# Kernel tuning notes

Measured on AMD Instinct MI355X. Metric: run time of the kernel, lower is better.

## Reference

```python
import jax, jax.numpy as jnp
import numpy as np

L, B, S, D, H, V = 6, 4, 1024, 1024, 16, 32000
HD = D // H          # head_size = 64
F = 4 * D            # ffn hidden
EPS = 1e-5           # nn.LayerNorm default


def setup_inputs() -> dict:
    key = jax.random.key(0)
    ks = jax.random.split(key, 12)
    s = 0.02
    p = {
        "tokens": jax.random.randint(ks[0], (B, S), 0, V, dtype=jnp.int32),
        "tok_emb": s * jax.random.normal(ks[1], (V, D), jnp.float32),
        "pos_emb": s * jax.random.normal(ks[2], (S, D), jnp.float32),
        # stacked per-layer params (leading dim L)
        "Wq": s * jax.random.normal(ks[3], (L, D, D), jnp.float32),
        "Wk": s * jax.random.normal(ks[4], (L, D, D), jnp.float32),
        "Wv": s * jax.random.normal(ks[5], (L, D, D), jnp.float32),
        "Wp": s * jax.random.normal(ks[6], (L, D, D), jnp.float32),
        "ln1_s": jnp.ones((L, D), jnp.float32),
        "ln1_b": jnp.zeros((L, D), jnp.float32),
        "W1": s * jax.random.normal(ks[7], (L, D, F), jnp.float32),
        "b1": jnp.zeros((L, F), jnp.float32),
        "W2": s * jax.random.normal(ks[8], (L, F, D), jnp.float32),
        "b2": jnp.zeros((L, D), jnp.float32),
        "ln2_s": jnp.ones((L, D), jnp.float32),
        "ln2_b": jnp.zeros((L, D), jnp.float32),
        "lnf_s": jnp.ones((D,), jnp.float32),
        "lnf_b": jnp.zeros((D,), jnp.float32),
        "Wh": s * jax.random.normal(ks[9], (D, V), jnp.float32),
        "bh": jnp.zeros((V,), jnp.float32),
    }
    return p


def _ln(x, scale, bias):
    m = x.mean(-1, keepdims=True)
    v = ((x - m) ** 2).mean(-1, keepdims=True)
    return (x - m) * jax.lax.rsqrt(v + EPS) * scale + bias


def reference(tokens, tok_emb, pos_emb, Wq, Wk, Wv, Wp, ln1_s, ln1_b,
              W1, b1, W2, b2, ln2_s, ln2_b, lnf_s, lnf_b, Wh, bh):
    x = tok_emb[tokens] + pos_emb[None, :, :]            # [B,S,D]
    mask = jnp.tril(jnp.ones((S, S), dtype=bool))
    inv_sqrt_hd = HD ** -0.5

    def layer(x, p):
        wq, wk, wv, wp, l1s, l1b, w1, b1_, w2, b2_, l2s, l2b = p
        q = jnp.einsum('bsd,dhk->bhsk', x, wq.reshape(D, H, HD))
        k = jnp.einsum('bsd,dhk->bhsk', x, wk.reshape(D, H, HD))
        v = jnp.einsum('bsd,dhk->bhsk', x, wv.reshape(D, H, HD))
        scores = jnp.einsum('bhsk,bhtk->bhst', q, k)     # [B,H,S,S]
        # original: masked_fill(-inf) THEN * head_size**-0.5 (same math: -inf stays -inf)
        scores = jnp.where(mask, scores * inv_sqrt_hd, -jnp.inf)
        attn = jax.nn.softmax(scores, axis=-1)
        o = jnp.einsum('bhst,bhtk->bhsk', attn, v)
        o = o.transpose(0, 2, 1, 3).reshape(B, S, D) @ wp
        a = x + _ln(o, l1s, l1b)                          # residual + ln1 (as in source)
        f = jax.nn.relu(a @ w1 + b1_) @ w2 + b2_
        return x + _ln(f, l2s, l2b), None                 # residual from block INPUT (as in source)

    x, _ = jax.lax.scan(layer, x,
                        (Wq, Wk, Wv, Wp, ln1_s, ln1_b, W1, b1, W2, b2, ln2_s, ln2_b))
    return _ln(x, lnf_s, lnf_b) @ Wh + bh                 # [B,S,V]
```

## Files before the change

kernel.cpp:

```cpp
#include <hip/hip_runtime.h>

#define DEV __device__ __forceinline__

typedef __attribute__((ext_vector_type(4))) float f32x4;
typedef __attribute__((ext_vector_type(8))) short short8_t;

constexpr int LNUM = 6;
constexpr int BB = 4;
constexpr int SS = 1024;
constexpr int DD = 1024;
constexpr int HH = 16;
constexpr int HDD = 64;
constexpr int FF = 4096;
constexpr int VV = 32000;
constexpr int MROWS = BB * SS;

DEV short f2bf(float f) {
  union { float f; unsigned u; } x; x.f = f;
  unsigned r = x.u + 0x7fffu + ((x.u >> 16) & 1u);
  return (short)(r >> 16);
}

DEV float bf2f(short s) {
  union { unsigned u; float f; } x;
  x.u = ((unsigned)(unsigned short)s) << 16;
  return x.f;
}

#define BAR() do { __builtin_amdgcn_sched_barrier(0); \
  __builtin_amdgcn_s_barrier(); \
  __builtin_amdgcn_sched_barrier(0); } while (0)

__global__ __launch_bounds__(256) void k_embed(
    const int* __restrict__ tok, const float* __restrict__ te,
    const float* __restrict__ pe, float* __restrict__ xf,
    short* __restrict__ xb) {
  int i = blockIdx.x * 256 + threadIdx.x;
  int bs = i >> 8, d4 = i & 255;
  int t = tok[bs];
  float4 a = ((const float4*)(te + (size_t)t * DD))[d4];
  float4 b = ((const float4*)(pe + (size_t)(bs & (SS - 1)) * DD))[d4];
  float4 r; r.x = a.x + b.x; r.y = a.y + b.y; r.z = a.z + b.z; r.w = a.w + b.w;
  ((float4*)xf)[i] = r;
  short4 o; o.x = f2bf(r.x); o.y = f2bf(r.y); o.z = f2bf(r.z); o.w = f2bf(r.w);
  ((short4*)xb)[i] = o;
}

__global__ __launch_bounds__(256) void k_tcvt4(
    const float* __restrict__ in, short* __restrict__ out, int K, int N,
    long long istride, long long ostride) {
  __shared__ float tile[64][65];
  const float* ip = in + (size_t)blockIdx.z * istride;
  short* op = out + (size_t)blockIdx.z * ostride;
  const int bn = blockIdx.x * 64, bk = blockIdx.y * 64;
  const int tc = threadIdx.x & 15, tr = threadIdx.x >> 4;
  #pragma unroll
  for (int i = 0; i < 4; i++) {
    const int r = tr + 16 * i;
    float4 v = *(const float4*)&ip[(size_t)(bk + r) * N + bn + tc * 4];
    tile[r][tc * 4 + 0] = v.x; tile[r][tc * 4 + 1] = v.y;
    tile[r][tc * 4 + 2] = v.z; tile[r][tc * 4 + 3] = v.w;
  }
  __syncthreads();
  #pragma unroll
  for (int i = 0; i < 4; i++) {
    const int wr = tr + 16 * i;
    short4 s;
    s.x = f2bf(tile[tc * 4 + 0][wr]);
    s.y = f2bf(tile[tc * 4 + 1][wr]);
    s.z = f2bf(tile[tc * 4 + 2][wr]);
    s.w = f2bf(tile[tc * 4 + 3][wr]);
    *(short4*)&op[(size_t)(bn + wr) * K + bk + tc * 4] = s;
  }
}

__global__ __launch_bounds__(256) void k_tcvt4q(
    const float* __restrict__ Wq, const float* __restrict__ Wk,
    const float* __restrict__ Wv, short* __restrict__ out) {
  __shared__ float tile[64][65];
  const int z = blockIdx.z, l = z / 3, which = z - l * 3;
  const float* ip = (which == 0 ? Wq : which == 1 ? Wk : Wv)
                    + (size_t)l * DD * DD;
  short* op = out + (size_t)z * DD * DD;
  const int bn = blockIdx.x * 64, bk = blockIdx.y * 64;
  const int tc = threadIdx.x & 15, tr = threadIdx.x >> 4;
  #pragma unroll
  for (int i = 0; i < 4; i++) {
    const int r = tr + 16 * i;
    float4 v = *(const float4*)&ip[(size_t)(bk + r) * DD + bn + tc * 4];
    tile[r][tc * 4 + 0] = v.x; tile[r][tc * 4 + 1] = v.y;
    tile[r][tc * 4 + 2] = v.z; tile[r][tc * 4 + 3] = v.w;
  }
  __syncthreads();
  #pragma unroll
  for (int i = 0; i < 4; i++) {
    const int wr = tr + 16 * i;
    short4 s;
    s.x = f2bf(tile[tc * 4 + 0][wr]);
    s.y = f2bf(tile[tc * 4 + 1][wr]);
    s.z = f2bf(tile[tc * 4 + 2][wr]);
    s.w = f2bf(tile[tc * 4 + 3][wr]);
    *(short4*)&op[(size_t)(bn + wr) * DD + bk + tc * 4] = s;
  }
}

DEV void gload16(const short* g, short* l) {
  __builtin_amdgcn_global_load_lds(
      (const __attribute__((address_space(1))) void*)g,
      (__attribute__((address_space(3))) void*)l, 16, 0, 0);
}

template<int MODE>
DEV void gemm256_body(short* lds,
    const short* __restrict__ A, const short* __restrict__ Bt,
    const float* __restrict__ bias, void* __restrict__ Cp,
    int M, int N, int K, int lda, int ldb) {
  const int tid = threadIdx.x;
  const int nbx = gridDim.x;
  const int nwg = nbx << 4;
  const int hid = blockIdx.y * nbx + blockIdx.x;
  const int cpx = nwg >> 3;
  const int lid = (hid & 7) * cpx + (hid >> 3);
  const int bx = lid >> 4, by = lid & 15;
  const int n0 = bx * 256, m0 = by * 256;

  const int lane = tid & 63;
  const int wid = tid >> 6;
  const int wm = wid >> 2, wn = wid & 3;
  const int l16 = lane & 15, kg = lane >> 4;
  const int xorv = (l16 & 7) << 4;
  const int cs[2] = { ((kg << 4) ^ xorv) >> 1,
                      ((64 | (kg << 4)) ^ xorv) >> 1 };
  const int rr = tid >> 3;
  const int sce = ((((tid & 7) << 4) ^ ((rr & 7) << 4)) >> 1);
  const int ldst = (tid & ~63) * 8;

  const int NT = K >> 6;

  auto stageA = [&](int t2, int c2) {
    const int k0 = t2 << 6;
    const int base = c2 * 32768;
    #pragma unroll
    for (int h = 0; h < 2; h++)
      #pragma unroll
      for (int li = 0; li < 2; li++)
        gload16(A + (size_t)(m0 + h * 128 + li * 64 + rr) * lda + k0 + sce,
                &lds[base + h * 8192 + li * 4096 + ldst]);
  };
  auto stageB = [&](int t2, int c2) {
    const int k0 = t2 << 6;
    const int base = c2 * 32768 + 16384;
    #pragma unroll
    for (int h = 0; h < 2; h++)
      #pragma unroll
      for (int li = 0; li < 2; li++)
        gload16(Bt + (size_t)(n0 + h * 128 + li * 64 + rr) * ldb + k0 + sce,
                &lds[base + h * 8192 + li * 4096 + ldst]);
  };

  f32x4 acc[8][4];
  #pragma unroll
  for (int mi = 0; mi < 8; mi++)
    #pragma unroll
    for (int ni = 0; ni < 4; ni++)
      #pragma unroll
      for (int j = 0; j < 4; j++) acc[mi][ni][j] = 0.f;

  auto storeQ = [&](int mlo, int nlo) {
    #pragma unroll
    for (int mi = 0; mi < 4; mi++)
      #pragma unroll
      for (int ni = 0; ni < 2; ni++)
        #pragma unroll
        for (int j = 0; j < 4; j++) {
          const int r = m0 + wm * 128 + (mlo + mi) * 16 + kg * 4 + j;
          const int c = n0 + wn * 64 + (nlo + ni) * 16 + l16;
          ((float*)Cp)[(size_t)r * N + c] = acc[mlo + mi][nlo + ni][j] + bias[c];
        }
  };

  stageA(0, 0); stageB(0, 0);
  stageA(1, 1); stageB(1, 1);
  asm volatile("s_waitcnt vmcnt(8)" ::: "memory");
  BAR();

  for (int t = 0; t < NT; t++) {
    const int c = t & 1;
    const int ao = c * 32768 + wm * 8192;
    const int bo = c * 32768 + 16384 + (wn >> 1) * 8192 + (wn & 1) * 4096;
    short8_t a[4][2], b0[2][2], b1[2][2];

    #pragma unroll
    for (int mi = 0; mi < 4; mi++)
      #pragma unroll
      for (int kk = 0; kk < 2; kk++)
        a[mi][kk] = *(const short8_t*)&lds[ao + (mi * 16 + l16) * 64 + cs[kk]];
    #pragma unroll
    for (int ni = 0; ni < 2; ni++)
      #pragma unroll
      for (int kk = 0; kk < 2; kk++)
        b0[ni][kk] = *(const short8_t*)&lds[bo + (ni * 16 + l16) * 64 + cs[kk]];
    BAR();
    __builtin_amdgcn_s_setprio(1);
    #pragma unroll
    for (int mi = 0; mi < 4; mi++)
      #pragma unroll
      for (int ni = 0; ni < 2; ni++)
        #pragma unroll
        for (int kk = 0; kk < 2; kk++)
          acc[mi][ni] = __builtin_amdgcn_mfma_f32_16x16x32_bf16(
              a[mi][kk], b0[ni][kk], acc[mi][ni], 0, 0, 0);
    __builtin_amdgcn_s_setprio(0);
    if (MODE == 9 && t == NT - 1) storeQ(0, 0);
    BAR();

    #pragma unroll
    for (int ni = 0; ni < 2; ni++)
      #pragma unroll
      for (int kk = 0; kk < 2; kk++)
        b1[ni][kk] = *(const short8_t*)&lds[bo + ((ni + 2) * 16 + l16) * 64 + cs[kk]];
    BAR();
    __builtin_amdgcn_s_setprio(1);
    #pragma unroll
    for (int mi = 0; mi < 4; mi++)
      #pragma unroll
      for (int ni = 0; ni < 2; ni++)
        #pragma unroll
        for (int kk = 0; kk < 2; kk++)
          acc[mi][ni + 2] = __builtin_amdgcn_mfma_f32_16x16x32_bf16(
              a[mi][kk], b1[ni][kk], acc[mi][ni + 2], 0, 0, 0);
    __builtin_amdgcn_s_setprio(0);
    if (MODE == 9 && t == NT - 1) storeQ(0, 2);
    BAR();

    #pragma unroll
    for (int mi = 0; mi < 4; mi++)
      #pragma unroll
      for (int kk = 0; kk < 2; kk++)
        a[mi][kk] = *(const short8_t*)&lds[ao + ((mi + 4) * 16 + l16) * 64 + cs[kk]];
    if (t + 2 < NT) stageB(t + 2, c);
    BAR();
    __builtin_amdgcn_s_setprio(1);
    #pragma unroll
    for (int mi = 0; mi < 4; mi++)
      #pragma unroll
      for (int ni = 0; ni < 2; ni++)
        #pragma unroll
        for (int kk = 0; kk < 2; kk++)
          acc[mi + 4][ni + 2] = __builtin_amdgcn_mfma_f32_16x16x32_bf16(
              a[mi][kk], b1[ni][kk], acc[mi + 4][ni + 2], 0, 0, 0);
    __builtin_amdgcn_s_setprio(0);
    if (MODE == 9 && t == NT - 1) storeQ(4, 2);
    BAR();

    if (t + 2 < NT) stageA(t + 2, c);
    BAR();
    __builtin_amdgcn_s_setprio(1);
    #pragma unroll
    for (int mi = 0; mi < 4; mi++)
      #pragma unroll
      for (int ni = 0; ni < 2; ni++)
        #pragma unroll
        for (int kk = 0; kk < 2; kk++)
          acc[mi + 4][ni] = __builtin_amdgcn_mfma_f32_16x16x32_bf16(
              a[mi][kk], b0[ni][kk], acc[mi + 4][ni], 0, 0, 0);
    __builtin_amdgcn_s_setprio(0);
    if (t + 2 < NT) asm volatile("s_waitcnt vmcnt(8)" ::: "memory");
    else            asm volatile("s_waitcnt vmcnt(0)" ::: "memory");
    BAR();
  }

  if (MODE == 9) {
    storeQ(4, 0);
    return;
  }
  #pragma unroll
  for (int mi = 0; mi < 8; mi++) {
    #pragma unroll
    for (int ni = 0; ni < 4; ni++) {
      #pragma unroll
      for (int j = 0; j < 4; j++) {
        const int r = m0 + wm * 128 + mi * 16 + kg * 4 + j;
        const int c = n0 + wn * 64 + ni * 16 + l16;
        const float v = acc[mi][ni][j];
        if (MODE == 6) {
          ((short*)Cp)[(size_t)r * N + c] = f2bf(fmaxf(v + bias[c], 0.f));
        } else if (MODE == 8) {
          int kind = c >> 10, cc = c & 1023;
          int b = r >> 10, s = r & 1023, h = cc >> 6, hd = cc & 63;
          size_t off;
          if (kind < 2)
            off = (size_t)kind * MROWS * DD +
                  (((size_t)(b * HH + h) << 10) + s) * HDD + hd;
          else
            off = (size_t)2 * MROWS * DD +
                  (((size_t)(b * HH + h) * HDD + hd) << 10) + s;
          ((short*)Cp)[off] = f2bf(v);
        }
      }
    }
  }
}

__global__ __launch_bounds__(512, 2) void k_qkv(
    const short* __restrict__ A, const short* __restrict__ Bt,
    const float* __restrict__ bias, void* __restrict__ Cp,
    int M, int N, int K, int lda, int ldb) {
  extern __shared__ short lds[];
  gemm256_body<8>(lds, A, Bt, bias, Cp, M, N, K, lda, ldb);
}
__global__ __launch_bounds__(512, 2) void k_ffn1(
    const short* __restrict__ A, const short* __restrict__ Bt,
    const float* __restrict__ bias, void* __restrict__ Cp,
    int M, int N, int K, int lda, int ldb) {
  extern __shared__ short lds[];
  gemm256_body<6>(lds, A, Bt, bias, Cp, M, N, K, lda, ldb);
}
__global__ __launch_bounds__(512, 2) void k_logits(
    const short* __restrict__ A, const short* __restrict__ Bt,
    const float* __restrict__ bias, void* __restrict__ Cp,
    int M, int N, int K, int lda, int ldb) {
  extern __shared__ short lds[];
  gemm256_body<9>(lds, A, Bt, bias, Cp, M, N, K, lda, ldb);
}

template<int MODE>
DEV void gemm128db_body(short* lds,
    const short* __restrict__ A, const short* __restrict__ Bt,
    const float* __restrict__ bias, void* __restrict__ Cp,
    int M, int N, int K, int lda, int ldb) {
  const int tid = threadIdx.x;
  const int n0 = blockIdx.x * 128, m0 = blockIdx.y * 128;
  const int lane = tid & 63;
  const int wid = tid >> 6;
  const int wm = wid >> 1, wn = wid & 1;
  const int l16 = lane & 15, kg = lane >> 4;
  const int xorv = (l16 & 7) << 4;
  const int cs[2] = { ((kg << 4) ^ xorv) >> 1,
                      ((64 | (kg << 4)) ^ xorv) >> 1 };
  const int rr = tid >> 3;
  const int sce = ((((tid & 7) << 4) ^ ((rr & 7) << 4)) >> 1);
  const int ldst = (tid & ~63) * 8;

  const int NT = K >> 6;

  auto stage = [&](int t2, int c2) {
    const int k0 = t2 << 6;
    const int base = c2 * 16384;
    #pragma unroll
    for (int i = 0; i < 4; i++)
      gload16(A + (size_t)(m0 + i * 32 + rr) * lda + k0 + sce,
              &lds[base + i * 2048 + ldst]);
    #pragma unroll
    for (int i = 0; i < 4; i++)
      gload16(Bt + (size_t)(n0 + i * 32 + rr) * ldb + k0 + sce,
              &lds[base + 8192 + i * 2048 + ldst]);
  };

  f32x4 acc[4][4];
  #pragma unroll
  for (int a = 0; a < 4; a++)
    #pragma unroll
    for (int b = 0; b < 4; b++)
      #pragma unroll
      for (int j = 0; j < 4; j++) acc[a][b][j] = 0.f;

  stage(0, 0);
  asm volatile("s_waitcnt vmcnt(0)" ::: "memory");
  BAR();

  for (int t = 0; t < NT; t++) {
    const int c = t & 1;
    if (t + 1 < NT) stage(t + 1, c ^ 1);
    const int ab = c * 16384;
    short8_t a[4][2], b[4][2];
    #pragma unroll
    for (int mi = 0; mi < 4; mi++)
      #pragma unroll
      for (int kk = 0; kk < 2; kk++)
        a[mi][kk] = *(const short8_t*)
            &lds[ab + (wm * 64 + mi * 16 + l16) * 64 + cs[kk]];
    #pragma unroll
    for (int ni = 0; ni < 4; ni++)
      #pragma unroll
      for (int kk = 0; kk < 2; kk++)
        b[ni][kk] = *(const short8_t*)
            &lds[ab + 8192 + (wn * 64 + ni * 16 + l16) * 64 + cs[kk]];
    __builtin_amdgcn_s_setprio(1);
    #pragma unroll
    for (int mi = 0; mi < 4; mi++)
      #pragma unroll
      for (int ni = 0; ni < 4; ni++)
        #pragma unroll
        for (int kk = 0; kk < 2; kk++)
          acc[mi][ni] = __builtin_amdgcn_mfma_f32_16x16x32_bf16(
              a[mi][kk], b[ni][kk], acc[mi][ni], 0, 0, 0);
    __builtin_amdgcn_s_setprio(0);
    if (t + 1 < NT) asm volatile("s_waitcnt vmcnt(0)" ::: "memory");
    BAR();
  }

  #pragma unroll
  for (int mi = 0; mi < 4; mi++) {
    #pragma unroll
    for (int ni = 0; ni < 4; ni++) {
      #pragma unroll
      for (int j = 0; j < 4; j++) {
        const int r = m0 + wm * 64 + mi * 16 + kg * 4 + j;
        const int c = n0 + wn * 64 + ni * 16 + l16;
        const float v = acc[mi][ni][j];
        if (MODE == 15) {
          ((short*)Cp)[(size_t)r * N + c] = f2bf(v);
        } else if (MODE == 17) {
          ((short*)Cp)[(size_t)r * N + c] = f2bf(v + bias[c]);
        }
      }
    }
  }
}

__global__ __launch_bounds__(256, 2) void k_proj(
    const short* __restrict__ A, const short* __restrict__ Bt,
    const float* __restrict__ bias, void* __restrict__ Cp,
    int M, int N, int K, int lda, int ldb) {
  extern __shared__ short lds[];
  gemm128db_body<15>(lds, A, Bt, bias, Cp, M, N, K, lda, ldb);
}
__global__ __launch_bounds__(256, 2) void k_ffn2(
    const short* __restrict__ A, const short* __restrict__ Bt,
    const float* __restrict__ bias, void* __restrict__ Cp,
    int M, int N, int K, int lda, int ldb) {
  extern __shared__ short lds[];
  gemm128db_body<17>(lds, A, Bt, bias, Cp, M, N, K, lda, ldb);
}

#define RDSWZ(arr, r, cb) \
  (*(const short8_t*)&arr[((r) << 6) + ((((cb) ^ (((r) & 7) << 4))) >> 1)])
#define RDSWZ7(arr, r, cb) \
  (*(const short8_t*)&arr[((r) << 7) + ((((cb) ^ (((r) & 7) << 4))) >> 1)])

__global__ __launch_bounds__(512, 2) void k_attn(
    const short* __restrict__ Qg, const short* __restrict__ Kgl,
    const short* __restrict__ Vt, short* __restrict__ Og) {
  extern __shared__ short sm[];
  short* lP = sm + 32768;
  const int tid = threadIdx.x;
  const int z = blockIdx.y;
  const int qb = (z < 32) ? blockIdx.x : 7 - blockIdx.x;
  const int q0 = qb << 7;
  const short* Qp = Qg + ((size_t)z << 16);
  const short* Kp = Kgl + ((size_t)z << 16);
  const short* Vp = Vt + ((size_t)z << 16);
  const int bidx = z >> 4, h = z & 15;
  const int lane = tid & 63, w = tid >> 6;
  const int l16 = lane & 15, kg = lane >> 4;
  const int sr = tid >> 3;
  const int scb = ((((tid & 7) << 4) ^ ((sr & 7) << 4)) >> 1);
  const int vr = tid >> 4;
  const int vcb = ((((tid & 15) << 4) ^ ((vr & 7) << 4)) >> 1);
  const int ldst = (tid & ~63) << 3;

  auto stageK = [&](int kt, int c) {
    const int k0 = kt << 7;
    short* dst = sm + c * 16384;
    #pragma unroll
    for (int i = 0; i < 2; i++)
      gload16(Kp + ((size_t)(k0 + i * 64 + sr) << 6) + scb,
              dst + i * 4096 + ldst);
  };
  auto stageV = [&](int kt, int c) {
    const int k0 = kt << 7;
    short* dst = sm + c * 16384 + 8192;
    #pragma unroll
    for (int i = 0; i < 2; i++)
      gload16(Vp + ((size_t)(i * 32 + vr) << 10) + k0 + vcb,
              dst + i * 4096 + ldst);
  };

  #pragma unroll
  for (int i = 0; i < 2; i++)
    gload16(Qp + ((size_t)(q0 + i * 64 + sr) << 6) + scb,
            sm + 16384 + i * 4096 + ldst);
  __syncthreads();
  short8_t aq[2];
  #pragma unroll
  for (int kk = 0; kk < 2; kk++)
    aq[kk] = RDSWZ((sm + 16384), w * 16 + l16, kk * 64 + kg * 16);
  __syncthreads();

  f32x4 acc_o[4];
  float m_r[4], l_r[4];
  #pragma unroll
  for (int j = 0; j < 4; j++) {
    m_r[j] = -3e38f; l_r[j] = 0.f;
    #pragma unroll
    for (int n2 = 0; n2 < 4; n2++) acc_o[n2][j] = 0.f;
  }

  const float C = 0.125f * 1.44269504f;
  const int nkt = qb + 1;
  stageK(0, 0); stageV(0, 0);

  for (int kt = 0; kt < nkt; kt++) {
    const int cur = kt & 1;
    if (kt + 1 < nkt) {
      stageK(kt + 1, cur ^ 1); stageV(kt + 1, cur ^ 1);
      asm volatile("s_waitcnt vmcnt(4)" ::: "memory");
    } else {
      asm volatile("s_waitcnt vmcnt(0)" ::: "memory");
    }
    BAR();

    const short* lK = sm + cur * 16384;
    const short* lV = sm + cur * 16384 + 8192;
    const int k0 = kt << 7;

    f32x4 s[8];
    #pragma unroll
    for (int nf = 0; nf < 8; nf++)
      #pragma unroll
      for (int j = 0; j < 4; j++) s[nf][j] = 0.f;
    #pragma unroll
    for (int kk = 0; kk < 2; kk++)
      #pragma unroll
      for (int nf = 0; nf < 8; nf++) {
        short8_t bk = RDSWZ(lK, nf * 16 + l16, kk * 64 + kg * 16);
        s[nf] = __builtin_amdgcn_mfma_f32_16x16x32_bf16(aq[kk], bk, s[nf], 0, 0, 0);
      }

    const bool diag = (kt == qb);
    #pragma unroll
    for (int j = 0; j < 4; j++) {
      const int ql = w * 16 + kg * 4 + j;
      const int q = q0 + ql;
      float sv[8]; float tm = -3e38f;
      #pragma unroll
      for (int nf = 0; nf < 8; nf++) {
        const int kv = k0 + nf * 16 + l16;
        const float x = s[nf][j] * C;
        sv[nf] = (!diag || kv <= q) ? x : -3e38f;
        tm = fmaxf(tm, sv[nf]);
      }
      #pragma unroll
      for (int o = 1; o < 16; o <<= 1) tm = fmaxf(tm, __shfl_xor(tm, o));
      const float mn = fmaxf(m_r[j], tm);
      const float scale = exp2f(m_r[j] - mn);
      float ts = 0.f;
      #pragma unroll
      for (int nf = 0; nf < 8; nf++) {
        const float e = exp2f(sv[nf] - mn);
        ts += e;
        lP[(ql << 7) + ((nf * 16 + l16) ^ ((ql & 7) << 3))] = f2bf(e);
      }
      #pragma unroll
      for (int o = 1; o < 16; o <<= 1) ts += __shfl_xor(ts, o);
      l_r[j] = l_r[j] * scale + ts;
      m_r[j] = mn;
      #pragma unroll
      for (int n2 = 0; n2 < 4; n2++) acc_o[n2][j] *= scale;
    }

    #pragma unroll
    for (int kc = 0; kc < 4; kc++) {
      const int pr = w * 16 + l16;
      short8_t pa = *(const short8_t*)
          &lP[(pr << 7) + ((kc * 32 + kg * 8) ^ ((pr & 7) << 3))];
      #pragma unroll
      for (int n2 = 0; n2 < 4; n2++) {
        short8_t vb = RDSWZ7(lV, n2 * 16 + l16, kc * 64 + kg * 16);
        acc_o[n2] = __builtin_amdgcn_mfma_f32_16x16x32_bf16(pa, vb, acc_o[n2], 0, 0, 0);
      }
    }
    BAR();
  }

  #pragma unroll
  for (int j = 0; j < 4; j++) {
    const int q = q0 + w * 16 + kg * 4 + j;
    const float inv = 1.f / l_r[j];
    #pragma unroll
    for (int n2 = 0; n2 < 4; n2++) {
      const int col = h * HDD + n2 * 16 + l16;
      Og[(((size_t)bidx << 10) + q) * DD + col] = f2bf(acc_o[n2][j] * inv);
    }
  }
}

template<int SRCB16, int ADD_RES, int WRITE_F32>
__global__ __launch_bounds__(256) void k_ln(
    const void* __restrict__ src, const float* __restrict__ res,
    const float* __restrict__ g, const float* __restrict__ b,
    float* __restrict__ of, short* __restrict__ ob) {
  const int row = blockIdx.x;
  const int tid = threadIdx.x;
  float4 v;
  if (SRCB16) {
    short4 s = ((const short4*)src)[((size_t)row << 8) + tid];
    v.x = bf2f(s.x); v.y = bf2f(s.y); v.z = bf2f(s.z); v.w = bf2f(s.w);
  } else {
    v = ((const float4*)src)[((size_t)row << 8) + tid];
  }
  float s1 = v.x + v.y + v.z + v.w;
  float s2 = v.x * v.x + v.y * v.y + v.z * v.z + v.w * v.w;
  #pragma unroll
  for (int o = 32; o; o >>= 1) { s1 += __shfl_xor(s1, o); s2 += __shfl_xor(s2, o); }
  __shared__ float sh1[4], sh2[4];
  if ((tid & 63) == 0) { sh1[tid >> 6] = s1; sh2[tid >> 6] = s2; }
  __syncthreads();
  s1 = sh1[0] + sh1[1] + sh1[2] + sh1[3];
  s2 = sh2[0] + sh2[1] + sh2[2] + sh2[3];
  const float mean = s1 * (1.f / 1024.f);
  const float var  = s2 * (1.f / 1024.f) - mean * mean;
  const float rs = rsqrtf(var + 1e-5f);
  float4 gg = ((const float4*)g)[tid];
  float4 bb = ((const float4*)b)[tid];
  float4 o4;
  o4.x = (v.x - mean) * rs * gg.x + bb.x;
  o4.y = (v.y - mean) * rs * gg.y + bb.y;
  o4.z = (v.z - mean) * rs * gg.z + bb.z;
  o4.w = (v.w - mean) * rs * gg.w + bb.w;
  if (ADD_RES) {
    float4 rr = ((const float4*)(res + ((size_t)row << 10)))[tid];
    o4.x += rr.x; o4.y += rr.y; o4.z += rr.z; o4.w += rr.w;
  }
  if (WRITE_F32) ((float4*)(of + ((size_t)row << 10)))[tid] = o4;
  short4 s4; s4.x = f2bf(o4.x); s4.y = f2bf(o4.y);
  s4.z = f2bf(o4.z); s4.w = f2bf(o4.w);
  ((short4*)ob)[((size_t)row << 8) + tid] = s4;
}

extern "C" void kernel_launch(void* const* d_in, const int* in_sizes, int n_in,
                              void* d_out, int out_size, void* d_ws, size_t ws_size,
                              hipStream_t stream) {
  (void)in_sizes; (void)n_in; (void)out_size; (void)ws_size;
  const int*   tokens  = (const int*)d_in[0];
  const float* tok_emb = (const float*)d_in[1];
  const float* pos_emb = (const float*)d_in[2];
  const float* Wq = (const float*)d_in[3];
  const float* Wk = (const float*)d_in[4];
  const float* Wv = (const float*)d_in[5];
  const float* Wp = (const float*)d_in[6];
  const float* ln1s = (const float*)d_in[7];
  const float* ln1b = (const float*)d_in[8];
  const float* W1 = (const float*)d_in[9];
  const float* b1 = (const float*)d_in[10];
  const float* W2 = (const float*)d_in[11];
  const float* b2 = (const float*)d_in[12];
  const float* ln2s = (const float*)d_in[13];
  const float* ln2b = (const float*)d_in[14];
  const float* lnfs = (const float*)d_in[15];
  const float* lnfb = (const float*)d_in[16];
  const float* Wh = (const float*)d_in[17];
  const float* bh = (const float*)d_in[18];
  float* out = (float*)d_out;

  hipFuncSetAttribute((const void*)k_qkv,
      hipFuncAttributeMaxDynamicSharedMemorySize, 131072);
  hipFuncSetAttribute((const void*)k_ffn1,
      hipFuncAttributeMaxDynamicSharedMemorySize, 131072);
  hipFuncSetAttribute((const void*)k_logits,
      hipFuncAttributeMaxDynamicSharedMemorySize, 131072);
  hipFuncSetAttribute((const void*)k_proj,
      hipFuncAttributeMaxDynamicSharedMemorySize, 65536);
  hipFuncSetAttribute((const void*)k_ffn2,
      hipFuncAttributeMaxDynamicSharedMemorySize, 65536);
  hipFuncSetAttribute((const void*)k_attn,
      hipFuncAttributeMaxDynamicSharedMemorySize, 98304);

  char* p = (char*)d_ws;
  auto alloc = [&](size_t elems, size_t esz) -> char* {
    char* r = p; p += (elems * esz + 255) & ~(size_t)255; return r;
  };
  short* WqkvT = (short*)alloc((size_t)LNUM * 3 * DD * DD, 2);
  short* WpT = (short*)alloc((size_t)LNUM * DD * DD, 2);
  short* W1T = (short*)alloc((size_t)LNUM * DD * FF, 2);
  short* W2T = (short*)alloc((size_t)LNUM * DD * FF, 2);
  short* WhT = (short*)alloc((size_t)DD * VV, 2);
  float* xf   = (float*)alloc((size_t)MROWS * DD, 4);
  short* ffb  = (short*)alloc((size_t)MROWS * DD, 2);
  short* xb   = (short*)alloc((size_t)MROWS * DD, 2);
  short* ab   = (short*)alloc((size_t)MROWS * DD, 2);
  short* qkvb = (short*)alloc((size_t)3 * MROWS * DD, 2);
  short* obuf = (short*)alloc((size_t)MROWS * DD, 2);
  short* hb   = (short*)alloc((size_t)MROWS * FF, 2);
  short* xfb  = (short*)alloc((size_t)MROWS * DD, 2);
  short* qb   = qkvb;
  short* kb   = qkvb + (size_t)MROWS * DD;
  short* vtb  = qkvb + (size_t)2 * MROWS * DD;

  dim3 blk(256);
  const long long DD2 = (long long)DD * DD;
  const long long DF  = (long long)DD * FF;
  k_tcvt4q<<<dim3(16, 16, 3 * LNUM), blk, 0, stream>>>(Wq, Wk, Wv, WqkvT);
  k_tcvt4<<<dim3(16, 16, LNUM), blk, 0, stream>>>(Wp, WpT, DD, DD, DD2, DD2);
  k_tcvt4<<<dim3(64, 16, LNUM), blk, 0, stream>>>(W1, W1T, DD, FF, DF, DF);
  k_tcvt4<<<dim3(16, 64, LNUM), blk, 0, stream>>>(W2, W2T, FF, DD, DF, DF);
  k_tcvt4<<<dim3(500, 16, 1),  blk, 0, stream>>>(Wh, WhT, DD, VV, 0, 0);

  k_embed<<<(MROWS * DD / 4) / 256, blk, 0, stream>>>(tokens, tok_emb, pos_emb, xf, xb);

  for (int l = 0; l < LNUM; l++) {
    const short* wqkv = WqkvT + (size_t)l * 3 * DD * DD;
    const short* wp = WpT + (size_t)l * DD * DD;
    const short* w1 = W1T + (size_t)l * DD * FF;
    const short* w2 = W2T + (size_t)l * DD * FF;

    k_qkv<<<dim3(12, 16), 512, 131072, stream>>>(xb, wqkv, nullptr, qkvb,
        MROWS, 3 * DD, DD, DD, DD);
    k_attn<<<dim3(8, BB * HH), 512, 98304, stream>>>(qb, kb, vtb, obuf);
    k_proj<<<dim3(8, 32), blk, 65536, stream>>>(obuf, wp, nullptr, ffb,
        MROWS, DD, DD, DD, DD);
    k_ln<1, 1, 0><<<MROWS, blk, 0, stream>>>(ffb, xf, ln1s + (size_t)l * DD,
        ln1b + (size_t)l * DD, nullptr, ab);
    k_ffn1<<<dim3(16, 16), 512, 131072, stream>>>(ab, w1, b1 + (size_t)l * FF, hb,
        MROWS, FF, DD, DD, DD);
    k_ffn2<<<dim3(8, 32), blk, 65536, stream>>>(hb, w2, b2 + (size_t)l * DD, ffb,
        MROWS, DD, FF, FF, FF);
    k_ln<1, 1, 1><<<MROWS, blk, 0, stream>>>(ffb, xf, ln2s + (size_t)l * DD,
        ln2b + (size_t)l * DD, xf, xb);
  }

  k_ln<0, 0, 0><<<MROWS, blk, 0, stream>>>(xf, nullptr, lnfs, lnfb, nullptr, xfb);
  k_logits<<<dim3(VV / 256, 16), 512, 131072, stream>>>(xfb, WhT, bh, out,
      MROWS, VV, DD, DD, DD);
}
```

Before: 2.010 ms.

## Replace 256x256 GEMM kernel with swizzled 128x128 tile GEMM for QKV, FFN1, logits

Removes the 512-thread 256x256-tile GEMM body. The QKV, FFN1 and logits projections now use the existing 256-thread 128x128 double-buffered GEMM, extended with their epilogues (head-split QKV store, bias+ReLU bf16, fp32 bias store). An optional block-index swizzle is added to group workgroups for L2 reuse. Smaller tiles give more workgroups and lower LDS use per block, at the cost of less operand reuse per tile. The staggered early stores of the logits path are also dropped.

New measurement: 2.152 ms. 7.1% more time.

```diff
diff --git a/kernel.cpp b/kernel.cpp
--- a/kernel.cpp
+++ b/kernel.cpp
@@ -110,227 +110,22 @@
       (__attribute__((address_space(3))) void*)l, 16, 0, 0);
 }
 
-template<int MODE>
-DEV void gemm256_body(short* lds,
-    const short* __restrict__ A, const short* __restrict__ Bt,
-    const float* __restrict__ bias, void* __restrict__ Cp,
-    int M, int N, int K, int lda, int ldb) {
-  const int tid = threadIdx.x;
-  const int nbx = gridDim.x;
-  const int nwg = nbx << 4;
-  const int hid = blockIdx.y * nbx + blockIdx.x;
-  const int cpx = nwg >> 3;
-  const int lid = (hid & 7) * cpx + (hid >> 3);
-  const int bx = lid >> 4, by = lid & 15;
-  const int n0 = bx * 256, m0 = by * 256;
-
-  const int lane = tid & 63;
-  const int wid = tid >> 6;
-  const int wm = wid >> 2, wn = wid & 3;
-  const int l16 = lane & 15, kg = lane >> 4;
-  const int xorv = (l16 & 7) << 4;
-  const int cs[2] = { ((kg << 4) ^ xorv) >> 1,
-                      ((64 | (kg << 4)) ^ xorv) >> 1 };
-  const int rr = tid >> 3;
-  const int sce = ((((tid & 7) << 4) ^ ((rr & 7) << 4)) >> 1);
-  const int ldst = (tid & ~63) * 8;
-
-  const int NT = K >> 6;
-
-  auto stageA = [&](int t2, int c2) {
-    const int k0 = t2 << 6;
-    const int base = c2 * 32768;
-    #pragma unroll
-    for (int h = 0; h < 2; h++)
-      #pragma unroll
-      for (int li = 0; li < 2; li++)
-        gload16(A + (size_t)(m0 + h * 128 + li * 64 + rr) * lda + k0 + sce,
-                &lds[base + h * 8192 + li * 4096 + ldst]);
-  };
-  auto stageB = [&](int t2, int c2) {
-    const int k0 = t2 << 6;
-    const int base = c2 * 32768 + 16384;
-    #pragma unroll
-    for (int h = 0; h < 2; h++)
-      #pragma unroll
-      for (int li = 0; li < 2; li++)
-        gload16(Bt + (size_t)(n0 + h * 128 + li * 64 + rr) * ldb + k0 + sce,
-                &lds[base + h * 8192 + li * 4096 + ldst]);
-  };
-
-  f32x4 acc[8][4];
-  #pragma unroll
-  for (int mi = 0; mi < 8; mi++)
-    #pragma unroll
-    for (int ni = 0; ni < 4; ni++)
-      #pragma unroll
-      for (int j = 0; j < 4; j++) acc[mi][ni][j] = 0.f;
-
-  auto storeQ = [&](int mlo, int nlo) {
-    #pragma unroll
-    for (int mi = 0; mi < 4; mi++)
-      #pragma unroll
-      for (int ni = 0; ni < 2; ni++)
-        #pragma unroll
-        for (int j = 0; j < 4; j++) {
-          const int r = m0 + wm * 128 + (mlo + mi) * 16 + kg * 4 + j;
-          const int c = n0 + wn * 64 + (nlo + ni) * 16 + l16;
-          ((float*)Cp)[(size_t)r * N + c] = acc[mlo + mi][nlo + ni][j] + bias[c];
-        }
-  };
-
-  stageA(0, 0); stageB(0, 0);
-  stageA(1, 1); stageB(1, 1);
-  asm volatile("s_waitcnt vmcnt(8)" ::: "memory");
-  BAR();
-
-  for (int t = 0; t < NT; t++) {
-    const int c = t & 1;
-    const int ao = c * 32768 + wm * 8192;
-    const int bo = c * 32768 + 16384 + (wn >> 1) * 8192 + (wn & 1) * 4096;
-    short8_t a[4][2], b0[2][2], b1[2][2];
-
-    #pragma unroll
-    for (int mi = 0; mi < 4; mi++)
-      #pragma unroll
-      for (int kk = 0; kk < 2; kk++)
-        a[mi][kk] = *(const short8_t*)&lds[ao + (mi * 16 + l16) * 64 + cs[kk]];
-    #pragma unroll
-    for (int ni = 0; ni < 2; ni++)
-      #pragma unroll
-      for (int kk = 0; kk < 2; kk++)
-        b0[ni][kk] = *(const short8_t*)&lds[bo + (ni * 16 + l16) * 64 + cs[kk]];
-    BAR();
-    __builtin_amdgcn_s_setprio(1);
-    #pragma unroll
-    for (int mi = 0; mi < 4; mi++)
-      #pragma unroll
-      for (int ni = 0; ni < 2; ni++)
-        #pragma unroll
-        for (int kk = 0; kk < 2; kk++)
-          acc[mi][ni] = __builtin_amdgcn_mfma_f32_16x16x32_bf16(
-              a[mi][kk], b0[ni][kk], acc[mi][ni], 0, 0, 0);
-    __builtin_amdgcn_s_setprio(0);
-    if (MODE == 9 && t == NT - 1) storeQ(0, 0);
-    BAR();
-
-    #pragma unroll
-    for (int ni = 0; ni < 2; ni++)
-      #pragma unroll
-      for (int kk = 0; kk < 2; kk++)
-        b1[ni][kk] = *(const short8_t*)&lds[bo + ((ni + 2) * 16 + l16) * 64 + cs[kk]];
-    BAR();
-    __builtin_amdgcn_s_setprio(1);
-    #pragma unroll
-    for (int mi = 0; mi < 4; mi++)
-      #pragma unroll
-      for (int ni = 0; ni < 2; ni++)
-        #pragma unroll
-        for (int kk = 0; kk < 2; kk++)
-          acc[mi][ni + 2] = __builtin_amdgcn_mfma_f32_16x16x32_bf16(
-              a[mi][kk], b1[ni][kk], acc[mi][ni + 2], 0, 0, 0);
-    __builtin_amdgcn_s_setprio(0);
-    if (MODE == 9 && t == NT - 1) storeQ(0, 2);
-    BAR();
-
-    #pragma unroll
-    for (int mi = 0; mi < 4; mi++)
-      #pragma unroll
-      for (int kk = 0; kk < 2; kk++)
-        a[mi][kk] = *(const short8_t*)&lds[ao + ((mi + 4) * 16 + l16) * 64 + cs[kk]];
-    if (t + 2 < NT) stageB(t + 2, c);
-    BAR();
-    __builtin_amdgcn_s_setprio(1);
-    #pragma unroll
-    for (int mi = 0; mi < 4; mi++)
-      #pragma unroll
-      for (int ni = 0; ni < 2; ni++)
-        #pragma unroll
-        for (int kk = 0; kk < 2; kk++)
-          acc[mi + 4][ni + 2] = __builtin_amdgcn_mfma_f32_16x16x32_bf16(
-              a[mi][kk], b1[ni][kk], acc[mi + 4][ni + 2], 0, 0, 0);
-    __builtin_amdgcn_s_setprio(0);
-    if (MODE == 9 && t == NT - 1) storeQ(4, 2);
-    BAR();
-
-    if (t + 2 < NT) stageA(t + 2, c);
-    BAR();
-    __builtin_amdgcn_s_setprio(1);
-    #pragma unroll
-    for (int mi = 0; mi < 4; mi++)
-      #pragma unroll
-      for (int ni = 0; ni < 2; ni++)
-        #pragma unroll
-        for (int kk = 0; kk < 2; kk++)
-          acc[mi + 4][ni] = __builtin_amdgcn_mfma_f32_16x16x32_bf16(
-              a[mi][kk], b0[ni][kk], acc[mi + 4][ni], 0, 0, 0);
-    __builtin_amdgcn_s_setprio(0);
-    if (t + 2 < NT) asm volatile("s_waitcnt vmcnt(8)" ::: "memory");
-    else            asm volatile("s_waitcnt vmcnt(0)" ::: "memory");
-    BAR();
-  }
-
-  if (MODE == 9) {
-    storeQ(4, 0);
-    return;
-  }
-  #pragma unroll
-  for (int mi = 0; mi < 8; mi++) {
-    #pragma unroll
-    for (int ni = 0; ni < 4; ni++) {
-      #pragma unroll
-      for (int j = 0; j < 4; j++) {
-        const int r = m0 + wm * 128 + mi * 16 + kg * 4 + j;
-        const int c = n0 + wn * 64 + ni * 16 + l16;
-        const float v = acc[mi][ni][j];
-        if (MODE == 6) {
-          ((short*)Cp)[(size_t)r * N + c] = f2bf(fmaxf(v + bias[c], 0.f));
-        } else if (MODE == 8) {
-          int kind = c >> 10, cc = c & 1023;
-          int b = r >> 10, s = r & 1023, h = cc >> 6, hd = cc & 63;
-          size_t off;
-          if (kind < 2)
-            off = (size_t)kind * MROWS * DD +
-                  (((size_t)(b * HH + h) << 10) + s) * HDD + hd;
-          else
-            off = (size_t)2 * MROWS * DD +
-                  (((size_t)(b * HH + h) * HDD + hd) << 10) + s;
-          ((short*)Cp)[off] = f2bf(v);
-        }
-      }
-    }
-  }
-}
-
-__global__ __launch_bounds__(512, 2) void k_qkv(
-    const short* __restrict__ A, const short* __restrict__ Bt,
-    const float* __restrict__ bias, void* __restrict__ Cp,
-    int M, int N, int K, int lda, int ldb) {
-  extern __shared__ short lds[];
-  gemm256_body<8>(lds, A, Bt, bias, Cp, M, N, K, lda, ldb);
-}
-__global__ __launch_bounds__(512, 2) void k_ffn1(
-    const short* __restrict__ A, const short* __restrict__ Bt,
-    const float* __restrict__ bias, void* __restrict__ Cp,
-    int M, int N, int K, int lda, int ldb) {
-  extern __shared__ short lds[];
-  gemm256_body<6>(lds, A, Bt, bias, Cp, M, N, K, lda, ldb);
-}
-__global__ __launch_bounds__(512, 2) void k_logits(
-    const short* __restrict__ A, const short* __restrict__ Bt,
-    const float* __restrict__ bias, void* __restrict__ Cp,
-    int M, int N, int K, int lda, int ldb) {
-  extern __shared__ short lds[];
-  gemm256_body<9>(lds, A, Bt, bias, Cp, M, N, K, lda, ldb);
-}
-
-template<int MODE>
+template<int MODE, int SWZ>
 DEV void gemm128db_body(short* lds,
     const short* __restrict__ A, const short* __restrict__ Bt,
     const float* __restrict__ bias, void* __restrict__ Cp,
     int M, int N, int K, int lda, int ldb) {
   const int tid = threadIdx.x;
-  const int n0 = blockIdx.x * 128, m0 = blockIdx.y * 128;
+  int bx = blockIdx.x, by = blockIdx.y;
+  if (SWZ) {
+    const int nbx = gridDim.x;
+    const int nwg = nbx << 5;
+    const int hid = by * nbx + bx;
+    const int cpx = nwg >> 3;
+    const int lid = (hid & 7) * cpx + (hid >> 3);
+    by = lid & 31; bx = lid >> 5;
+  }
+  const int n0 = bx * 128, m0 = by * 128;
   const int lane = tid & 63;
   const int wid = tid >> 6;
   const int wm = wid >> 1, wn = wid & 1;
@@ -413,25 +208,61 @@
           ((short*)Cp)[(size_t)r * N + c] = f2bf(v);
         } else if (MODE == 17) {
           ((short*)Cp)[(size_t)r * N + c] = f2bf(v + bias[c]);
+        } else if (MODE == 6) {
+          ((short*)Cp)[(size_t)r * N + c] = f2bf(fmaxf(v + bias[c], 0.f));
+        } else if (MODE == 9) {
+          ((float*)Cp)[(size_t)r * N + c] = v + bias[c];
+        } else if (MODE == 8) {
+          int kind = c >> 10, cc = c & 1023;
+          int b2 = r >> 10, s = r & 1023, h = cc >> 6, hd = cc & 63;
+          size_t off;
+          if (kind < 2)
+            off = (size_t)kind * MROWS * DD +
+                  (((size_t)(b2 * HH + h) << 10) + s) * HDD + hd;
+          else
+            off = (size_t)2 * MROWS * DD +
+                  (((size_t)(b2 * HH + h) * HDD + hd) << 10) + s;
+          ((short*)Cp)[off] = f2bf(v);
         }
       }
     }
   }
 }
 
+__global__ __launch_bounds__(256, 2) void k_qkv(
+    const short* __restrict__ A, const short* __restrict__ Bt,
+    const float* __restrict__ bias, void* __restrict__ Cp,
+    int M, int N, int K, int lda, int ldb) {
+  extern __shared__ short lds[];
+  gemm128db_body<8, 1>(lds, A, Bt, bias, Cp, M, N, K, lda, ldb);
+}
+__global__ __launch_bounds__(256, 2) void k_ffn1(
+    const short* __restrict__ A, const short* __restrict__ Bt,
+    const float* __restrict__ bias, void* __restrict__ Cp,
+    int M, int N, int K, int lda, int ldb) {
+  extern __shared__ short lds[];
+  gemm128db_body<6, 1>(lds, A, Bt, bias, Cp, M, N, K, lda, ldb);
+}
+__global__ __launch_bounds__(256, 2) void k_logits(
+    const short* __restrict__ A, const short* __restrict__ Bt,
+    const float* __restrict__ bias, void* __restrict__ Cp,
+    int M, int N, int K, int lda, int ldb) {
+  extern __shared__ short lds[];
+  gemm128db_body<9, 1>(lds, A, Bt, bias, Cp, M, N, K, lda, ldb);
+}
 __global__ __launch_bounds__(256, 2) void k_proj(
     const short* __restrict__ A, const short* __restrict__ Bt,
     const float* __restrict__ bias, void* __restrict__ Cp,
     int M, int N, int K, int lda, int ldb) {
   extern __shared__ short lds[];
-  gemm128db_body<15>(lds, A, Bt, bias, Cp, M, N, K, lda, ldb);
+  gemm128db_body<15, 0>(lds, A, Bt, bias, Cp, M, N, K, lda, ldb);
 }
 __global__ __launch_bounds__(256, 2) void k_ffn2(
     const short* __restrict__ A, const short* __restrict__ Bt,
     const float* __restrict__ bias, void* __restrict__ Cp,
     int M, int N, int K, int lda, int ldb) {
   extern __shared__ short lds[];
-  gemm128db_body<17>(lds, A, Bt, bias, Cp, M, N, K, lda, ldb);
+  gemm128db_body<17, 0>(lds, A, Bt, bias, Cp, M, N, K, lda, ldb);
 }
 
 #define RDSWZ(arr, r, cb) \
@@ -655,11 +486,11 @@
   float* out = (float*)d_out;
 
   hipFuncSetAttribute((const void*)k_qkv,
-      hipFuncAttributeMaxDynamicSharedMemorySize, 131072);
+      hipFuncAttributeMaxDynamicSharedMemorySize, 65536);
   hipFuncSetAttribute((const void*)k_ffn1,
-      hipFuncAttributeMaxDynamicSharedMemorySize, 131072);
+      hipFuncAttributeMaxDynamicSharedMemorySize, 65536);
   hipFuncSetAttribute((const void*)k_logits,
-      hipFuncAttributeMaxDynamicSharedMemorySize, 131072);
+      hipFuncAttributeMaxDynamicSharedMemorySize, 65536);
   hipFuncSetAttribute((const void*)k_proj,
       hipFuncAttributeMaxDynamicSharedMemorySize, 65536);
   hipFuncSetAttribute((const void*)k_ffn2,
@@ -705,14 +536,14 @@
     const short* w1 = W1T + (size_t)l * DD * FF;
     const short* w2 = W2T + (size_t)l * DD * FF;
 
-    k_qkv<<<dim3(12, 16), 512, 131072, stream>>>(xb, wqkv, nullptr, qkvb,
+    k_qkv<<<dim3(24, 32), blk, 65536, stream>>>(xb, wqkv, nullptr, qkvb,
         MROWS, 3 * DD, DD, DD, DD);
     k_attn<<<dim3(8, BB * HH), 512, 98304, stream>>>(qb, kb, vtb, obuf);
     k_proj<<<dim3(8, 32), blk, 65536, stream>>>(obuf, wp, nullptr, ffb,
         MROWS, DD, DD, DD, DD);
     k_ln<1, 1, 0><<<MROWS, blk, 0, stream>>>(ffb, xf, ln1s + (size_t)l * DD,
         ln1b + (size_t)l * DD, nullptr, ab);
-    k_ffn1<<<dim3(16, 16), 512, 131072, stream>>>(ab, w1, b1 + (size_t)l * FF, hb,
+    k_ffn1<<<dim3(32, 32), blk, 65536, stream>>>(ab, w1, b1 + (size_t)l * FF, hb,
         MROWS, FF, DD, DD, DD);
     k_ffn2<<<dim3(8, 32), blk, 65536, stream>>>(hb, w2, b2 + (size_t)l * DD, ffb,
         MROWS, DD, FF, FF, FF);
@@ -721,6 +552,6 @@
   }
 
   k_ln<0, 0, 0><<<MROWS, blk, 0, stream>>>(xf, nullptr, lnfs, lnfb, nullptr, xfb);
-  k_logits<<<dim3(VV / 256, 16), 512, 131072, stream>>>(xfb, WhT, bh, out,
+  k_logits<<<dim3(VV / 128, 32), blk, 65536, stream>>>(xfb, WhT, bh, out,
       MROWS, VV, DD, DD, DD);
 }
```
